# Kernel optimization log

Hardware: AMD Instinct MI355X
Metric: run time of the kernel (lower is better)

Reference implementation:

```python
import jax, jax.numpy as jnp
import numpy as np

SEQ, D, H = 4096, 1024, 16
HD = D // H
SCALE = HD ** -0.5


def setup_inputs() -> dict:
    key = jax.random.key(0)
    ks = jax.random.split(key, 8)
    s = 0.02
    return {
        "hidden_states": jax.random.normal(ks[0], (SEQ, D), dtype=jnp.float32),
        "wq": jax.random.normal(ks[1], (D, D), dtype=jnp.float32) * s,
        "bq": jax.random.normal(ks[2], (D,), dtype=jnp.float32) * s,
        "wk": jax.random.normal(ks[3], (D, D), dtype=jnp.float32) * s,
        "wv": jax.random.normal(ks[4], (D, D), dtype=jnp.float32) * s,
        "bv": jax.random.normal(ks[5], (D,), dtype=jnp.float32) * s,
        "wo": jax.random.normal(ks[6], (D, D), dtype=jnp.float32) * s,
        "bo": jax.random.normal(ks[7], (D,), dtype=jnp.float32) * s,
    }


def reference(hidden_states, wq, bq, wk, wv, bv, wo, bo):
    S = hidden_states.shape[0]
    # torch Linear: y = x @ W^T + b  (k_proj has no bias)
    q = (hidden_states @ wq.T + bq).reshape(S, H, HD).transpose(1, 0, 2)  # [H,S,hd]
    k = (hidden_states @ wk.T).reshape(S, H, HD).transpose(1, 0, 2)       # [H,S,hd]
    v = (hidden_states @ wv.T + bv).reshape(S, H, HD).transpose(1, 0, 2)  # [H,S,hd]
    scores = jnp.einsum('hqd,hkd->hqk', q, k) * SCALE                     # [H,S,S]
    # softmax computed in fp32 then cast back to query dtype
    attn = jax.nn.softmax(scores.astype(jnp.float32), axis=-1).astype(q.dtype)
    out = jnp.einsum('hqk,hkd->hqd', attn, v)                             # [H,S,hd]
    out = out.transpose(1, 0, 2).reshape(S, D)
    return out @ wo.T + bo
```

## Files before the change

### kernel.cpp

```cpp
#include <hip/hip_runtime.h>

#define SEQ 4096
#define DIM 1024
#define NH 16
#define HD 64
#define QKVSTR 3072

typedef __attribute__((ext_vector_type(8))) short bf16x8;
typedef __attribute__((ext_vector_type(4))) float f32x4;
typedef __attribute__((ext_vector_type(16))) float f32x16;
typedef __attribute__((ext_vector_type(4))) unsigned int uint4v;

__device__ __forceinline__ unsigned short f2bf(float f) {
  unsigned int b = __float_as_uint(f);
  b = b + 0x7fffu + ((b >> 16) & 1u);
  return (unsigned short)(b >> 16);
}

__device__ __forceinline__ unsigned int cvt_pk_bf16(float lo, float hi) {
  unsigned int r;
  asm("v_cvt_pk_bf16_f32 %0, %1, %2" : "=v"(r) : "v"(lo), "v"(hi));
  return r;
}

__device__ __forceinline__ float fast_exp2(float x) {
#if __has_builtin(__builtin_amdgcn_exp2f)
  return __builtin_amdgcn_exp2f(x);
#else
  float r; asm("v_exp_f32 %0, %1" : "=v"(r) : "v"(x)); return r;
#endif
}

typedef __attribute__((address_space(3))) unsigned int lds_uint;
typedef __attribute__((address_space(1))) const unsigned int global_uint;

__device__ __forceinline__ void gload_lds16(const void* g, void* l) {
  __builtin_amdgcn_global_load_lds((global_uint*)g, (lds_uint*)l, 16, 0, 0);
}

__global__ __launch_bounds__(256) void cast_all_kernel(
    const float* __restrict__ X, const float* __restrict__ wq, const float* __restrict__ wk,
    const float* __restrict__ wv, const float* __restrict__ wo,
    unsigned short* __restrict__ Xb, unsigned short* __restrict__ Wqkv,
    unsigned short* __restrict__ Wob, float qscale) {
  int i = blockIdx.x * 256 + threadIdx.x;
  const float* src;
  unsigned short* dst;
  float sc = 1.f;
  if (i < 524288) { src = X + (size_t)i * 8; dst = Xb + (size_t)i * 8; }
  else if (i < 655360) { int j = i - 524288; src = wq + (size_t)j * 8; dst = Wqkv + (size_t)j * 8; sc = qscale; }
  else if (i < 786432) { int j = i - 655360; src = wk + (size_t)j * 8; dst = Wqkv + 1048576 + (size_t)j * 8; }
  else if (i < 917504) { int j = i - 786432; src = wv + (size_t)j * 8; dst = Wqkv + 2097152 + (size_t)j * 8; }
  else { int j = i - 917504; src = wo + (size_t)j * 8; dst = Wob + (size_t)j * 8; }
  const float4* p = (const float4*)src;
  float4 x0 = p[0], x1 = p[1];
  union { unsigned short u[8]; uint4v v; } o;
  o.u[0] = f2bf(x0.x * sc); o.u[1] = f2bf(x0.y * sc);
  o.u[2] = f2bf(x0.z * sc); o.u[3] = f2bf(x0.w * sc);
  o.u[4] = f2bf(x1.x * sc); o.u[5] = f2bf(x1.y * sc);
  o.u[6] = f2bf(x1.z * sc); o.u[7] = f2bf(x1.w * sc);
  *(uint4v*)dst = o.v;
}

template<int BIASMODE, int OUT_F32>
__global__ __launch_bounds__(256) void gemm_bt_kernel(
    const unsigned short* __restrict__ A, const unsigned short* __restrict__ B,
    const float* __restrict__ b0, const float* __restrict__ b1, float qscale,
    void* __restrict__ Cout, int M, int N, int K) {
  __shared__ unsigned short As[128 * 32];
  __shared__ unsigned short Bs[128 * 32];
  int tid = threadIdx.x;
  int wave = tid >> 6, lane = tid & 63;
  int g = lane >> 4, lc = lane & 15;
  int wm = wave >> 1, wn = wave & 1;

  int gx = gridDim.x;
  int wgid = blockIdx.y * gx + blockIdx.x;
  int cpx = (gx * gridDim.y) >> 3;
  int sw = (wgid & 7) * cpx + (wgid >> 3);
  int m0 = (sw / gx) * 128, n0 = (sw % gx) * 128;

  f32x4 acc[4][4] = {};

  for (int k0 = 0; k0 < K; k0 += 32) {
    __syncthreads();
    for (int c = 0; c < 2; ++c) {
      int chunk = c * 256 + wave * 64 + lane;
      int row = chunk >> 2, cb = chunk & 3;
      gload_lds16(A + (size_t)(m0 + row) * K + k0 + cb * 8, As + (c * 256 + wave * 64) * 8);
      gload_lds16(B + (size_t)(n0 + row) * K + k0 + cb * 8, Bs + (c * 256 + wave * 64) * 8);
    }
    __syncthreads();
    bf16x8 af[4], bfr[4];
    for (int mf = 0; mf < 4; ++mf)
      af[mf] = *(const bf16x8*)&As[(wm * 64 + mf * 16 + lc) * 32 + g * 8];
    for (int nf = 0; nf < 4; ++nf)
      bfr[nf] = *(const bf16x8*)&Bs[(wn * 64 + nf * 16 + lc) * 32 + g * 8];
    for (int mf = 0; mf < 4; ++mf)
      for (int nf = 0; nf < 4; ++nf)
        acc[mf][nf] = __builtin_amdgcn_mfma_f32_16x16x32_bf16(af[mf], bfr[nf], acc[mf][nf], 0, 0, 0);
  }

  for (int nf = 0; nf < 4; ++nf) {
    int col = n0 + wn * 64 + nf * 16 + lc;
    float bias = 0.f;
    if (BIASMODE == 1) {
      int sect = col >> 10, cc = col & 1023;
      bias = (sect == 0) ? b0[cc] * qscale : ((sect == 2) ? b1[cc] : 0.f);
    } else if (BIASMODE == 2) {
      bias = b0[col];
    }
    for (int mf = 0; mf < 4; ++mf) {
      int row = m0 + wm * 64 + mf * 16 + g * 4;
      for (int r = 0; r < 4; ++r) {
        float v = acc[mf][nf][r] + bias;
        if (OUT_F32) ((float*)Cout)[(size_t)(row + r) * N + col] = v;
        else ((unsigned short*)Cout)[(size_t)(row + r) * N + col] = f2bf(v);
      }
    }
  }
}

__global__ __launch_bounds__(256) void transpose_kernel(
    const unsigned short* __restrict__ V, unsigned short* __restrict__ Vt) {
  __shared__ unsigned short Ts[64 * 72];
  int tid = threadIdx.x;
  int s0 = blockIdx.x * 64, d0 = blockIdx.y * 64;
  for (int c = 0; c < 2; ++c) {
    int q = c * 256 + tid;
    int r = q >> 3, cb = q & 7;
    uint4v v = *(const uint4v*)&V[(size_t)(s0 + r) * QKVSTR + d0 + cb * 8];
    *(uint4v*)&Ts[r * 72 + cb * 8] = v;
  }
  __syncthreads();
  for (int c = 0; c < 2; ++c) {
    int q = c * 256 + tid;
    int d = q >> 3, sc = q & 7;
    union { unsigned short u[8]; uint4v v; } ov;
    for (int j = 0; j < 8; ++j) ov.u[j] = Ts[(sc * 8 + j) * 72 + d];
    *(uint4v*)&Vt[(size_t)(d0 + d) * SEQ + s0 + sc * 8] = ov.v;
  }
}

__global__ __launch_bounds__(256) void attn_kernel(
    const unsigned short* __restrict__ QKV, const unsigned short* __restrict__ Vt,
    unsigned short* __restrict__ Aout) {
  __shared__ unsigned short Qs[128 * 64];
  __shared__ unsigned short Ks[2][64 * 64];
  __shared__ unsigned short Vs[2][64 * 64];
  int tid = threadIdx.x;
  int w = tid >> 6, lane = tid & 63;
  int hi = lane >> 5, l31 = lane & 31;

  int bid = blockIdx.x;
  int swz = (bid & 7) * 64 + (bid >> 3);
  int h = swz >> 5;
  int q0 = (swz & 31) * 128;

  const unsigned short* Qg = QKV + h * HD;
  const unsigned short* Kg = QKV + DIM + h * HD;
  const unsigned short* Vg = Vt + (size_t)(h * HD) * SEQ;

  int ch0 = w * 64 + lane;
  int r0s = ch0 >> 3, d0s = (ch0 & 7) ^ (r0s & 7);
  int ch1 = 256 + ch0;
  int r1s = ch1 >> 3, d1s = (ch1 & 7) ^ (r1s & 7);
  size_t koff0 = (size_t)r0s * QKVSTR + d0s * 8;
  size_t koff1 = (size_t)r1s * QKVSTR + d1s * 8;
  size_t voff0 = (size_t)r0s * SEQ + d0s * 8;
  size_t voff1 = (size_t)r1s * SEQ + d1s * 8;
  unsigned short* ldsK_lo[2] = { &Ks[0][(w * 64) * 8],       &Ks[1][(w * 64) * 8] };
  unsigned short* ldsK_hi[2] = { &Ks[0][(256 + w * 64) * 8], &Ks[1][(256 + w * 64) * 8] };
  unsigned short* ldsV_lo[2] = { &Vs[0][(w * 64) * 8],       &Vs[1][(w * 64) * 8] };
  unsigned short* ldsV_hi[2] = { &Vs[0][(256 + w * 64) * 8], &Vs[1][(256 + w * 64) * 8] };

  for (int c = 0; c < 4; ++c) {
    int chunk = c * 256 + w * 64 + lane;
    int row = chunk >> 3, pos = chunk & 7;
    int db = pos ^ (row & 7);
    gload_lds16(Qg + (size_t)(q0 + row) * QKVSTR + db * 8, Qs + (c * 256 + w * 64) * 8);
  }
  gload_lds16(Kg + koff0, ldsK_lo[0]);
  gload_lds16(Kg + koff1, ldsK_hi[0]);
  gload_lds16(Vg + voff0, ldsV_lo[0]);
  gload_lds16(Vg + voff1, ldsV_hi[0]);
  asm volatile("s_waitcnt vmcnt(4)" ::: "memory");
  __builtin_amdgcn_sched_barrier(0);
  __builtin_amdgcn_s_barrier();

  bf16x8 qf[4];
  {
    int qrow = w * 32 + l31;
    for (int dc = 0; dc < 4; ++dc) {
      int pos = 2 * dc + hi;
      qf[dc] = *(const bf16x8*)&Qs[qrow * 64 + (pos ^ (qrow & 7)) * 8];
    }
  }

  int offb[4];
#pragma unroll
  for (int dc = 0; dc < 4; ++dc)
    offb[dc] = l31 * 128 + (((2 * dc + hi) ^ (l31 & 7)) * 16);
  const char* KbA = (const char*)&Ks[0][0];
  const char* KbB = (const char*)&Ks[1][0];
  const char* VbA = (const char*)&Vs[0][0];
  const char* VbB = (const char*)&Vs[1][0];

  union { unsigned short us[8]; bf16x8 v; } one8;
#pragma unroll
  for (int j = 0; j < 8; ++j) one8.us[j] = 0x3F80;

  f32x16 o0 = {}, o1 = {}, lsa = {};
  int cur = 0;

  for (int t = 0; t < SEQ / 64; ++t) {
    {
      int kvn = ((t + 1) & (SEQ / 64 - 1)) * 64;
      const unsigned short* Kt = Kg + (size_t)kvn * QKVSTR;
      const unsigned short* Vtt = Vg + kvn;
      int nb = cur ^ 1;
      gload_lds16(Kt + koff0, ldsK_lo[nb]);
      gload_lds16(Kt + koff1, ldsK_hi[nb]);
      gload_lds16(Vtt + voff0, ldsV_lo[nb]);
      gload_lds16(Vtt + voff1, ldsV_hi[nb]);
    }
    asm volatile("s_waitcnt vmcnt(4)" ::: "memory");
    __builtin_amdgcn_sched_barrier(0);
    __builtin_amdgcn_s_barrier();
    __builtin_amdgcn_sched_barrier(0);

    const char* Kb = cur ? KbB : KbA;
    const char* Vb = cur ? VbB : VbA;

    bf16x8 kf0[4], kf1[4];
#pragma unroll
    for (int dc = 0; dc < 4; ++dc) {
      kf0[dc] = *(const bf16x8*)(Kb + offb[dc]);
      kf1[dc] = *(const bf16x8*)(Kb + offb[dc] + 4096);
    }
    f32x16 st0 = {}, st1 = {};
    __builtin_amdgcn_s_setprio(1);
#pragma unroll
    for (int dc = 0; dc < 4; ++dc) {
      st0 = __builtin_amdgcn_mfma_f32_32x32x16_bf16(kf0[dc], qf[dc], st0, 0, 0, 0);
      st1 = __builtin_amdgcn_mfma_f32_32x32x16_bf16(kf1[dc], qf[dc], st1, 0, 0, 0);
    }
    __builtin_amdgcn_s_setprio(0);

    bf16x8 vf0[4], vf1[4];
#pragma unroll
    for (int c = 0; c < 4; ++c) {
      vf0[c] = *(const bf16x8*)(Vb + offb[c]);
      vf1[c] = *(const bf16x8*)(Vb + offb[c] + 4096);
    }

    float p0[16], p1[16];
#pragma unroll
    for (int r = 0; r < 16; ++r) p0[r] = fast_exp2(st0[r]);
#pragma unroll
    for (int r = 0; r < 16; ++r) p1[r] = fast_exp2(st1[r]);

    bf16x8 pa[4];
#pragma unroll
    for (int f = 0; f < 2; ++f) {
      const float* pp = f ? p1 : p0;
#pragma unroll
      for (int cc = 0; cc < 2; ++cc) {
        unsigned uLO0 = cvt_pk_bf16(pp[8 * cc + 0], pp[8 * cc + 1]);
        unsigned uLO1 = cvt_pk_bf16(pp[8 * cc + 2], pp[8 * cc + 3]);
        unsigned uHI0 = cvt_pk_bf16(pp[8 * cc + 4], pp[8 * cc + 5]);
        unsigned uHI1 = cvt_pk_bf16(pp[8 * cc + 6], pp[8 * cc + 7]);
        auto s0 = __builtin_amdgcn_permlane32_swap(uLO0, uHI0, false, false);
        auto s1 = __builtin_amdgcn_permlane32_swap(uLO1, uHI1, false, false);
        union { unsigned u[4]; bf16x8 v; } pw;
        pw.u[0] = s0[0]; pw.u[1] = s1[0]; pw.u[2] = s0[1]; pw.u[3] = s1[1];
        pa[f * 2 + cc] = pw.v;
      }
    }

    __builtin_amdgcn_s_setprio(1);
#pragma unroll
    for (int c = 0; c < 4; ++c) {
      o0 = __builtin_amdgcn_mfma_f32_32x32x16_bf16(pa[c], vf0[c], o0, 0, 0, 0);
      o1 = __builtin_amdgcn_mfma_f32_32x32x16_bf16(pa[c], vf1[c], o1, 0, 0, 0);
      lsa = __builtin_amdgcn_mfma_f32_32x32x16_bf16(pa[c], one8.v, lsa, 0, 0, 0);
    }
    __builtin_amdgcn_s_setprio(0);

    asm volatile("" ::: "memory");
    __builtin_amdgcn_sched_barrier(0);
    __builtin_amdgcn_s_barrier();
    cur ^= 1;
  }

  float* Qf = (float*)Qs;
  if (l31 == 0) {
#pragma unroll
    for (int r = 0; r < 16; ++r)
      Qf[w * 32 + ((r & 3) + 8 * (r >> 2) + 4 * hi)] = lsa[r];
  }
  float inv = 1.f / Qf[w * 32 + l31];
#pragma unroll
  for (int r = 0; r < 16; ++r) {
    int qr = (r & 3) + 8 * (r >> 2) + 4 * hi;
    float ir = __shfl(inv, qr + (lane & 32));
    size_t row = q0 + w * 32 + qr;
    Aout[row * DIM + h * HD + l31]      = f2bf(o0[r] * ir);
    Aout[row * DIM + h * HD + 32 + l31] = f2bf(o1[r] * ir);
  }
}

extern "C" void kernel_launch(void* const* d_in, const int* in_sizes, int n_in,
                              void* d_out, int out_size, void* d_ws, size_t ws_size,
                              hipStream_t stream) {
  (void)in_sizes; (void)n_in; (void)out_size; (void)ws_size;
  const float* X  = (const float*)d_in[0];
  const float* wq = (const float*)d_in[1];
  const float* bq = (const float*)d_in[2];
  const float* wk = (const float*)d_in[3];
  const float* wv = (const float*)d_in[4];
  const float* bv = (const float*)d_in[5];
  const float* wo = (const float*)d_in[6];
  const float* bo = (const float*)d_in[7];

  char* ws = (char*)d_ws;
  const size_t SZ_XD  = (size_t)SEQ * DIM * 2;
  const size_t SZ_W   = (size_t)DIM * DIM * 2;
  const size_t SZ_QKV = (size_t)SEQ * QKVSTR * 2;
  unsigned short* Xb   = (unsigned short*)(ws);
  unsigned short* Wqkv = (unsigned short*)(ws + SZ_XD);
  unsigned short* Wob  = (unsigned short*)(ws + SZ_XD + 3 * SZ_W);
  unsigned short* QKVb = (unsigned short*)(ws + SZ_XD + 4 * SZ_W);
  unsigned short* Vtb  = (unsigned short*)(ws + SZ_XD + 4 * SZ_W + SZ_QKV);
  unsigned short* Ab   = Xb;

  const float QSCALE = 0.125f * 1.44269504088896f;

  cast_all_kernel<<<4096, 256, 0, stream>>>(X, wq, wk, wv, wo, Xb, Wqkv, Wob, QSCALE);

  gemm_bt_kernel<1, 0><<<dim3(QKVSTR / 128, SEQ / 128), 256, 0, stream>>>(
      Xb, Wqkv, bq, bv, QSCALE, QKVb, SEQ, QKVSTR, DIM);

  transpose_kernel<<<dim3(SEQ / 64, DIM / 64), 256, 0, stream>>>(QKVb + 2 * DIM, Vtb);

  attn_kernel<<<SEQ / 128 * NH, 256, 0, stream>>>(QKVb, Vtb, Ab);

  gemm_bt_kernel<2, 1><<<dim3(DIM / 128, SEQ / 128), 256, 0, stream>>>(
      Ab, Wob, bo, nullptr, 1.f, d_out, SEQ, DIM, DIM);
}
```

Before: 170.0 us.

## Double-buffer LDS tiles in GEMM to overlap global loads with MFMA

The bf16 GEMM kernel now keeps two LDS buffers for its A and B tiles. It issues the global-to-LDS loads for the next K-slice before computing on the current one. A vmcnt wait plus explicit barriers replace the two __syncthreads, so load latency can hide behind MFMA work. In exchange LDS use doubles, and one redundant wrap-around load is issued on the last iteration.

```diff
diff --git a/kernel.cpp b/kernel.cpp
--- a/kernel.cpp
+++ b/kernel.cpp
@@ -67,8 +67,8 @@
     const unsigned short* __restrict__ A, const unsigned short* __restrict__ B,
     const float* __restrict__ b0, const float* __restrict__ b1, float qscale,
     void* __restrict__ Cout, int M, int N, int K) {
-  __shared__ unsigned short As[128 * 32];
-  __shared__ unsigned short Bs[128 * 32];
+  __shared__ unsigned short As[2][128 * 32];
+  __shared__ unsigned short Bs[2][128 * 32];
   int tid = threadIdx.x;
   int wave = tid >> 6, lane = tid & 63;
   int g = lane >> 4, lc = lane & 15;
@@ -80,25 +80,54 @@
   int sw = (wgid & 7) * cpx + (wgid >> 3);
   int m0 = (sw / gx) * 128, n0 = (sw % gx) * 128;
 
+  int ch0 = wave * 64 + lane;
+  int r0 = ch0 >> 2, cb0 = ch0 & 3;
+  int ch1 = 256 + ch0;
+  int r1 = ch1 >> 2, cb1 = ch1 & 3;
+  const unsigned short* Ar0 = A + (size_t)(m0 + r0) * K + cb0 * 8;
+  const unsigned short* Ar1 = A + (size_t)(m0 + r1) * K + cb1 * 8;
+  const unsigned short* Br0 = B + (size_t)(n0 + r0) * K + cb0 * 8;
+  const unsigned short* Br1 = B + (size_t)(n0 + r1) * K + cb1 * 8;
+  unsigned short* sAlo[2] = { &As[0][(wave * 64) * 8],       &As[1][(wave * 64) * 8] };
+  unsigned short* sAhi[2] = { &As[0][(256 + wave * 64) * 8], &As[1][(256 + wave * 64) * 8] };
+  unsigned short* sBlo[2] = { &Bs[0][(wave * 64) * 8],       &Bs[1][(wave * 64) * 8] };
+  unsigned short* sBhi[2] = { &Bs[0][(256 + wave * 64) * 8], &Bs[1][(256 + wave * 64) * 8] };
+
   f32x4 acc[4][4] = {};
 
+  gload_lds16(Ar0, sAlo[0]);
+  gload_lds16(Ar1, sAhi[0]);
+  gload_lds16(Br0, sBlo[0]);
+  gload_lds16(Br1, sBhi[0]);
+
+  int cur = 0;
   for (int k0 = 0; k0 < K; k0 += 32) {
-    __syncthreads();
-    for (int c = 0; c < 2; ++c) {
-      int chunk = c * 256 + wave * 64 + lane;
-      int row = chunk >> 2, cb = chunk & 3;
-      gload_lds16(A + (size_t)(m0 + row) * K + k0 + cb * 8, As + (c * 256 + wave * 64) * 8);
-      gload_lds16(B + (size_t)(n0 + row) * K + k0 + cb * 8, Bs + (c * 256 + wave * 64) * 8);
-    }
-    __syncthreads();
+    {
+      int kn = (k0 + 32 < K) ? (k0 + 32) : 0;
+      int nb = cur ^ 1;
+      gload_lds16(Ar0 + kn, sAlo[nb]);
+      gload_lds16(Ar1 + kn, sAhi[nb]);
+      gload_lds16(Br0 + kn, sBlo[nb]);
+      gload_lds16(Br1 + kn, sBhi[nb]);
+    }
+    asm volatile("s_waitcnt vmcnt(4)" ::: "memory");
+    __builtin_amdgcn_sched_barrier(0);
+    __builtin_amdgcn_s_barrier();
+    __builtin_amdgcn_sched_barrier(0);
+
     bf16x8 af[4], bfr[4];
     for (int mf = 0; mf < 4; ++mf)
-      af[mf] = *(const bf16x8*)&As[(wm * 64 + mf * 16 + lc) * 32 + g * 8];
+      af[mf] = *(const bf16x8*)&As[cur][(wm * 64 + mf * 16 + lc) * 32 + g * 8];
     for (int nf = 0; nf < 4; ++nf)
-      bfr[nf] = *(const bf16x8*)&Bs[(wn * 64 + nf * 16 + lc) * 32 + g * 8];
+      bfr[nf] = *(const bf16x8*)&Bs[cur][(wn * 64 + nf * 16 + lc) * 32 + g * 8];
     for (int mf = 0; mf < 4; ++mf)
       for (int nf = 0; nf < 4; ++nf)
         acc[mf][nf] = __builtin_amdgcn_mfma_f32_16x16x32_bf16(af[mf], bfr[nf], acc[mf][nf], 0, 0, 0);
+
+    asm volatile("" ::: "memory");
+    __builtin_amdgcn_sched_barrier(0);
+    __builtin_amdgcn_s_barrier();
+    cur ^= 1;
   }
 
   for (int nf = 0; nf < 4; ++nf) {
```

Result: no change. 167.3 us (-1.6%).
